# Kernel tuning notes

Hardware: AMD Instinct MI355X
Metric: run time of the kernel (lower is better)

## Reference

```python
import jax, jax.numpy as jnp
import numpy as np

N_STATE = 2048
N_HEAD = 16
HEAD_DIM = N_STATE // N_HEAD  # 128
ROPE_THETA = 10000.0


def setup_inputs() -> dict:
    key = jax.random.key(0)
    ks = jax.random.split(key, 8)
    B, S, D = 2, 2048, N_STATE
    scale = 1.0 / np.sqrt(D)
    x = jax.random.normal(ks[0], (B, S, D), dtype=jnp.float32)
    Wq = jax.random.normal(ks[1], (D, D), dtype=jnp.float32) * scale
    bq = jnp.zeros((D,), dtype=jnp.float32)
    Wk = jax.random.normal(ks[2], (D, D), dtype=jnp.float32) * scale  # key has no bias
    Wv = jax.random.normal(ks[3], (D, D), dtype=jnp.float32) * scale
    bv = jnp.zeros((D,), dtype=jnp.float32)
    Wo = jax.random.normal(ks[4], (D, D), dtype=jnp.float32) * scale
    bo = jnp.zeros((D,), dtype=jnp.float32)
    return {"x": x, "Wq": Wq, "bq": bq, "Wk": Wk, "Wv": Wv, "bv": bv, "Wo": Wo, "bo": bo}


def _rope(t, pos):
    # t: [B, S, H, hd]; torchtune-style interleaved rotary (pairs of adjacent dims)
    hd = t.shape[-1]
    inv_freq = 1.0 / (ROPE_THETA ** (jnp.arange(0, hd, 2, dtype=jnp.float32) / hd))  # [hd/2]
    ang = pos[:, None] * inv_freq[None, :]                    # [S, hd/2]
    cos = jnp.cos(ang)[None, :, None, :].astype(t.dtype)       # [1,S,1,hd/2]
    sin = jnp.sin(ang)[None, :, None, :].astype(t.dtype)
    t1 = t[..., 0::2]
    t2 = t[..., 1::2]
    rot = jnp.stack([t1 * cos - t2 * sin, t2 * cos + t1 * sin], axis=-1)
    return rot.reshape(t.shape)


def reference(x, Wq, bq, Wk, Wv, bv, Wo, bo):
    B, S, D = x.shape
    H, hd = N_HEAD, D // N_HEAD
    q = (x @ Wq.T + bq).reshape(B, S, H, hd)
    k = (x @ Wk.T).reshape(B, S, H, hd)
    v = (x @ Wv.T + bv).reshape(B, S, H, hd)
    pos = jnp.arange(S, dtype=jnp.float32)
    q = _rope(q, pos)
    k = _rope(k, pos)
    # [B,H,S,hd]
    q = q.transpose(0, 2, 1, 3)
    k = k.transpose(0, 2, 1, 3)
    v = v.transpose(0, 2, 1, 3)
    scale = 1.0 / jnp.sqrt(jnp.asarray(hd, dtype=x.dtype))
    scores = jnp.einsum('bhqd,bhkd->bhqk', q, k) * scale       # [B,H,S,S]
    causal = jnp.tril(jnp.ones((S, S), dtype=bool))
    scores = jnp.where(causal[None, None], scores, jnp.finfo(scores.dtype).min)
    probs = jax.nn.softmax(scores, axis=-1)
    a = jnp.einsum('bhqk,bhkd->bhqd', probs, v)                # [B,H,S,hd]
    a = a.transpose(0, 2, 1, 3).reshape(B, S, D)
    return a @ Wo.T + bo
```

## Files before the change

kernel.cpp:

```cpp
#include <hip/hip_runtime.h>
#include <stdint.h>

typedef float f32x4 __attribute__((ext_vector_type(4)));
typedef __bf16 bf16x8 __attribute__((ext_vector_type(8)));
typedef unsigned short us8 __attribute__((ext_vector_type(8)));
typedef unsigned short us4 __attribute__((ext_vector_type(4)));
typedef unsigned int u32;

#define MFMA16(A, B, C) __builtin_amdgcn_mfma_f32_16x16x32_bf16( \
    __builtin_bit_cast(bf16x8, (A)), __builtin_bit_cast(bf16x8, (B)), (C), 0, 0, 0)

__device__ __forceinline__ unsigned short f2bf(float f) {
  u32 u = __builtin_bit_cast(u32, f);
  u = u + 0x7fffu + ((u >> 16) & 1u);
  return (unsigned short)(u >> 16);
}
__device__ __forceinline__ float bf2f(unsigned short b) {
  u32 u = ((u32)b) << 16;
  return __builtin_bit_cast(float, u);
}
__device__ __forceinline__ void gload16(const void* g, void* lds) {
  __builtin_amdgcn_global_load_lds((const __attribute__((address_space(1))) u32*)g,
                                   (__attribute__((address_space(3))) u32*)lds, 16, 0, 0);
}

__global__ __launch_bounds__(256) void convert_all(
    const float* __restrict__ x, const float* __restrict__ wq, const float* __restrict__ wk,
    const float* __restrict__ wv, const float* __restrict__ wo,
    unsigned short* __restrict__ xb, unsigned short* __restrict__ wcat,
    unsigned short* __restrict__ wob) {
  int tid = blockIdx.x * 256 + threadIdx.x;
  int nth = gridDim.x * 256;
  const float* srcs[5] = {x, wq, wk, wv, wo};
  unsigned short* dsts[5] = {xb, wcat, wcat + 4194304, wcat + 8388608, wob};
  const int n4s[5] = {2097152, 1048576, 1048576, 1048576, 1048576};
#pragma unroll
  for (int sg = 0; sg < 5; ++sg) {
    const float4* s = (const float4*)srcs[sg];
    us4* d = (us4*)dsts[sg];
    int n4 = n4s[sg];
    for (int i = tid; i < n4; i += nth) {
      float4 v = s[i];
      us4 o;
      o[0] = f2bf(v.x); o[1] = f2bf(v.y); o[2] = f2bf(v.z); o[3] = f2bf(v.w);
      d[i] = o;
    }
  }
}

template <int EPI>
__global__ __launch_bounds__(512, 2) void gemm2(
    const unsigned short* __restrict__ A, const unsigned short* __restrict__ B,
    int nTN, int N,
    float* __restrict__ outF, const float* __restrict__ bias,
    unsigned short* __restrict__ qb, unsigned short* __restrict__ kb,
    unsigned short* __restrict__ vtb, const float* __restrict__ bq,
    const float* __restrict__ bv) {
  constexpr int K = 2048, KT = 64;
  __shared__ alignas(16) char L[4 * 24576];
  int bid = (int)blockIdx.x, nwg = (int)gridDim.x;
  {
    int qq = nwg >> 3;
    int xcd = bid & 7, idx = bid >> 3;
    bid = xcd * qq + idx;
  }
  int tm = bid / nTN, tn = bid % nTN;
  int t = (int)threadIdx.x, l = t & 63, w = t >> 6;
  int g = l >> 4, ln = l & 15;
  int wr = w >> 2, wc = w & 3;
  const unsigned short* Ab =
      A + (size_t)(tm * 128 + w * 16 + (l >> 2)) * K + (l & 3) * 8;
  const unsigned short* Bb =
      B + (size_t)(tn * 256 + w * 16 + (l >> 2)) * K + (l & 3) * 8;
  f32x4 acc[4][4] = {};

#define STAGE(tile) do {                                                      \
    char* Lb = L + ((tile) & 3) * 24576 + w * 1024;                           \
    int kc = (tile) * 32;                                                     \
    gload16(Ab + kc, Lb);                                \
    gload16(Bb + kc, Lb + 8192);                         \
    gload16(Bb + (size_t)128 * K + kc, Lb + 16384);      \
  } while (0)

#define GITER(kt, VM) do {                                                    \
    asm volatile("s_waitcnt vmcnt(" #VM ")" ::: "memory");                    \
    __builtin_amdgcn_s_barrier();                                             \
    __builtin_amdgcn_sched_barrier(0);                                        \
    asm volatile("" ::: "memory");                                            \
    if ((kt) + 3 < KT) STAGE((kt) + 3);                                       \
    const unsigned short* Lc = (const unsigned short*)(L + ((kt) & 3) * 24576); \
    us8 af[4], bfr[4];                                                        \
    _Pragma("unroll") for (int mf = 0; mf < 4; ++mf)                          \
      af[mf] = *(const us8*)&Lc[(wr * 64 + mf * 16 + ln) * 32 + g * 8];       \
    _Pragma("unroll") for (int nf = 0; nf < 4; ++nf)                          \
      bfr[nf] = *(const us8*)&Lc[4096 + (wc * 64 + nf * 16 + ln) * 32 + g * 8]; \
    __builtin_amdgcn_s_setprio(1);                                            \
    _Pragma("unroll") for (int mf = 0; mf < 4; ++mf)                          \
      _Pragma("unroll") for (int nf = 0; nf < 4; ++nf)                        \
        acc[mf][nf] = MFMA16(af[mf], bfr[nf], acc[mf][nf]);                   \
    __builtin_amdgcn_s_setprio(0);                                            \
  } while (0)

  STAGE(0); STAGE(1); STAGE(2);
#pragma unroll 1
  for (int kt = 0; kt < KT - 2; ++kt) GITER(kt, 6);
  GITER(KT - 2, 3);
  GITER(KT - 1, 0);
#undef STAGE
#undef GITER

  if (EPI == 1) {
#pragma unroll
    for (int mf = 0; mf < 4; ++mf)
#pragma unroll
      for (int nf = 0; nf < 4; ++nf) {
        int n = tn * 256 + wc * 64 + nf * 16 + ln;
        float bz = bias[n];
#pragma unroll
        for (int r = 0; r < 4; ++r) {
          int m = tm * 128 + wr * 64 + mf * 16 + g * 4 + r;
          outF[(size_t)m * N + n] = acc[mf][nf][r] + bz;
        }
      }
  } else {
#pragma unroll
    for (int mf = 0; mf < 4; ++mf)
#pragma unroll
      for (int nf = 0; nf < 4; ++nf) {
        int n6 = tn * 256 + wc * 64 + nf * 16 + ln;
        int sel = n6 >> 11, d = n6 & 2047, h = d >> 7, hd = d & 127;
        int m0 = tm * 128 + wr * 64 + mf * 16 + g * 4;
        int b = m0 >> 11, s0 = m0 & 2047;
        if (sel == 2) {
          float badd = bv[d];
          us4 pk;
#pragma unroll
          for (int r = 0; r < 4; ++r) pk[r] = f2bf(acc[mf][nf][r] + badd);
          *(us4*)&vtb[((size_t)(b * 16 + h) * 128 + hd) * 2048 + s0] = pk;
        } else {
          unsigned short* dst = sel ? kb : qb;
          float badd = sel ? 0.f : bq[d];
#pragma unroll
          for (int r = 0; r < 4; ++r)
            dst[((size_t)(b * 16 + h) * 2048 + (s0 + r)) * 128 + hd] =
                f2bf(acc[mf][nf][r] + badd);
        }
      }
  }
}

__global__ __launch_bounds__(256) void rope_k(u32* __restrict__ q, u32* __restrict__ k) {
  int idx = blockIdx.x * 256 + threadIdx.x;
  int i = idx & 63;
  int s = (idx >> 6) & 2047;
  float ang = (float)s * exp2f(-(float)i * 0.2076205059304703f);
  float sv, cv;
  sincosf(ang, &sv, &cv);
  u32 qu = q[idx];
  float a0 = bf2f((unsigned short)(qu & 0xffff)), a1 = bf2f((unsigned short)(qu >> 16));
  q[idx] = (u32)f2bf(a0 * cv - a1 * sv) | ((u32)f2bf(a1 * cv + a0 * sv) << 16);
  u32 ku = k[idx];
  float b0 = bf2f((unsigned short)(ku & 0xffff)), b1 = bf2f((unsigned short)(ku >> 16));
  k[idx] = (u32)f2bf(b0 * cv - b1 * sv) | ((u32)f2bf(b1 * cv + b0 * sv) << 16);
}

__global__ __launch_bounds__(512) void attn_k(
    const unsigned short* __restrict__ qg, const unsigned short* __restrict__ kg,
    const unsigned short* __restrict__ vtg, unsigned short* __restrict__ ab) {
  __shared__ alignas(16) unsigned short Kl[64 * 128];
  __shared__ alignas(16) unsigned short Vl[128 * 64];
  __shared__ alignas(16) unsigned short Pl[8][16 * 72];
  int bh = (int)blockIdx.x & 31;
  int pr = (int)blockIdx.x >> 5;
  int t = (int)threadIdx.x, l = t & 63, w = t >> 6;
  int g = l >> 4, ln = l & 15;
  int b = bh >> 4, h = bh & 15;
  const size_t bq0 = (size_t)bh * 2048 * 128;

#pragma unroll 1
  for (int half = 0; half < 2; ++half) {
    int qt = half ? 15 - pr : pr;
    int qbase = qt * 128;
    int qrow = qbase + w * 16 + ln;
    us8 qf[4];
#pragma unroll
    for (int kf = 0; kf < 4; ++kf)
      qf[kf] = *(const us8*)&qg[bq0 + (size_t)qrow * 128 + kf * 32 + g * 8];
    f32x4 o[8] = {};
    float mrow = -1e30f, lrow = 0.f;
    int nkt = (qbase >> 6) + 2;
#pragma unroll 1
    for (int kt = 0; kt < nkt; ++kt) {
      __syncthreads();
#pragma unroll
      for (int i = 0; i < 2; ++i) {
        int fb = i * 8192 + w * 1024;
        int flat = fb + l * 16;
        int row = flat >> 8, colb = flat & 255;
        int sc = colb ^ ((row & 7) << 4);
        gload16(kg + (bq0 + (size_t)(kt * 64 + row) * 128 + (sc >> 1)), (char*)Kl + fb);
        int rv = flat >> 7, cv2 = flat & 127;
        int scv = cv2 ^ ((rv & 7) << 4);
        gload16(vtg + (bq0 + (size_t)rv * 2048 + kt * 64 + (scv >> 1)), (char*)Vl + fb);
      }
      __syncthreads();
      f32x4 st[4];
#pragma unroll
      for (int kfr = 0; kfr < 4; ++kfr) {
        f32x4 acc = {};
        int row = kfr * 16 + ln;
        int swz = (row & 7) << 4;
#pragma unroll
        for (int kf = 0; kf < 4; ++kf) {
          us8 kfrag = *(const us8*)((const char*)Kl + row * 256 + ((kf * 64 + g * 16) ^ swz));
          acc = MFMA16(kfrag, qf[kf], acc);
        }
        st[kfr] = acc;
      }
      float pmax = -1e30f;
#pragma unroll
      for (int kfr = 0; kfr < 4; ++kfr)
#pragma unroll
        for (int r = 0; r < 4; ++r) {
          int key = kt * 64 + kfr * 16 + g * 4 + r;
          float sv = key <= qrow ? st[kfr][r] * 0.08838834764831845f : -1e30f;
          st[kfr][r] = sv;
          pmax = fmaxf(pmax, sv);
        }
      pmax = fmaxf(pmax, __shfl_xor(pmax, 16));
      pmax = fmaxf(pmax, __shfl_xor(pmax, 32));
      if (__ballot(pmax > mrow + 8.f)) {
        float mnew = pmax > mrow + 8.f ? pmax : mrow;
        float corr = exp2f((mrow - mnew) * 1.44269504f);
        mrow = mnew;
        lrow *= corr;
#pragma unroll
        for (int r = 0; r < 4; ++r) {
          float cr = __shfl(corr, g * 4 + r);
#pragma unroll
          for (int nf = 0; nf < 8; ++nf) o[nf][r] *= cr;
        }
      }
      float lsum = 0.f;
#pragma unroll
      for (int kfr = 0; kfr < 4; ++kfr) {
        us4 pk;
#pragma unroll
        for (int r = 0; r < 4; ++r) {
          float p = exp2f((st[kfr][r] - mrow) * 1.44269504f);
          lsum += p;
          pk[r] = f2bf(p);
        }
        *(us4*)&Pl[w][ln * 72 + kfr * 16 + g * 4] = pk;
      }
      lsum += __shfl_xor(lsum, 16);
      lsum += __shfl_xor(lsum, 32);
      lrow += lsum;
#pragma unroll
      for (int kf2 = 0; kf2 < 2; ++kf2) {
        us8 pa = *(const us8*)&Pl[w][ln * 72 + kf2 * 32 + g * 8];
#pragma unroll
        for (int nf = 0; nf < 8; ++nf) {
          int row = nf * 16 + ln;
          us8 vb = *(const us8*)((const char*)Vl + row * 128 +
                                 ((kf2 * 64 + g * 16) ^ ((row & 7) << 4)));
          o[nf] = MFMA16(pa, vb, o[nf]);
        }
      }
    }
    float invl = 1.f / lrow;
#pragma unroll
    for (int r = 0; r < 4; ++r) {
      float ir = __shfl(invl, g * 4 + r);
      int srow = qbase + w * 16 + g * 4 + r;
      size_t base = ((size_t)b * 2048 + srow) * 2048 + h * 128 + ln;
#pragma unroll
      for (int nf = 0; nf < 8; ++nf) ab[base + (size_t)nf * 16] = f2bf(o[nf][r] * ir);
    }
  }
}

extern "C" void kernel_launch(void* const* d_in, const int* in_sizes, int n_in,
                              void* d_out, int out_size, void* d_ws, size_t ws_size,
                              hipStream_t stream) {
  const float* x  = (const float*)d_in[0];
  const float* Wq = (const float*)d_in[1];
  const float* bq = (const float*)d_in[2];
  const float* Wk = (const float*)d_in[3];
  const float* Wv = (const float*)d_in[4];
  const float* bv = (const float*)d_in[5];
  const float* Wo = (const float*)d_in[6];
  const float* bo = (const float*)d_in[7];
  float* out = (float*)d_out;

  unsigned short* ws = (unsigned short*)d_ws;
  unsigned short* xb   = ws;
  unsigned short* wcat = xb + 8388608;
  unsigned short* wob  = wcat + 12582912;
  unsigned short* qb   = wob + 4194304;
  unsigned short* kb   = qb + 8388608;
  unsigned short* vtb  = kb + 8388608;

  convert_all<<<2048, 256, 0, stream>>>(x, Wq, Wk, Wv, Wo, xb, wcat, wob);
  gemm2<0><<<768, 512, 0, stream>>>(xb, wcat, 24, 6144,
                                    nullptr, nullptr, qb, kb, vtb, bq, bv);
  rope_k<<<16384, 256, 0, stream>>>((u32*)qb, (u32*)kb);
  attn_k<<<256, 512, 0, stream>>>(qb, kb, vtb, xb );
  gemm2<1><<<256, 512, 0, stream>>>(xb, wob, 8, 2048,
                                    out, bo, nullptr, nullptr, nullptr, nullptr, nullptr);
}
```

Before: 284.4 us.

## Rewrite GEMM as 256x256 tiles with 8-phase double-buffered LDS pipeline

Replaces the 128x256-tile GEMM with a 256x256-tile kernel using K=64 per stage, double-buffered 128KB LDS, and an 8-phase schedule interleaving half-tile global loads with MFMA sub-blocks. This raises arithmetic intensity per loaded byte and overlaps loads with compute at finer granularity. It halves the grid (384 and 128 blocks), which can reduce occupancy on 256 CUs, and the 128KB LDS limits each CU to one block despite the launch bounds.

```diff
diff --git a/kernel.cpp b/kernel.cpp
--- a/kernel.cpp
+++ b/kernel.cpp
@@ -49,15 +49,16 @@
 }
 
 template <int EPI>
-__global__ __launch_bounds__(512, 2) void gemm2(
+__global__ __launch_bounds__(512, 2) void gemm8(
     const unsigned short* __restrict__ A, const unsigned short* __restrict__ B,
     int nTN, int N,
     float* __restrict__ outF, const float* __restrict__ bias,
     unsigned short* __restrict__ qb, unsigned short* __restrict__ kb,
     unsigned short* __restrict__ vtb, const float* __restrict__ bq,
     const float* __restrict__ bv) {
-  constexpr int K = 2048, KT = 64;
-  __shared__ alignas(16) char L[4 * 24576];
+  constexpr int KT = 32;
+  __shared__ alignas(16) char L[131072];
+  char* Lp = L;
   int bid = (int)blockIdx.x, nwg = (int)gridDim.x;
   {
     int qq = nwg >> 3;
@@ -68,84 +69,120 @@
   int t = (int)threadIdx.x, l = t & 63, w = t >> 6;
   int g = l >> 4, ln = l & 15;
   int wr = w >> 2, wc = w & 3;
-  const unsigned short* Ab =
-      A + (size_t)(tm * 128 + w * 16 + (l >> 2)) * K + (l & 3) * 8;
-  const unsigned short* Bb =
-      B + (size_t)(tn * 256 + w * 16 + (l >> 2)) * K + (l & 3) * 8;
-  f32x4 acc[4][4] = {};
-
-#define STAGE(tile) do {                                                      \
-    char* Lb = L + ((tile) & 3) * 24576 + w * 1024;                           \
-    int kc = (tile) * 32;                                                     \
-    gload16(Ab + kc, Lb);                                \
-    gload16(Bb + kc, Lb + 8192);                         \
-    gload16(Bb + (size_t)128 * K + kc, Lb + 16384);      \
+  const unsigned short* pA = A + (size_t)(tm * 256 + l) * 2048 + w * 8;
+  const unsigned short* pB = B + (size_t)(tn * 256 + l) * 2048 + w * 8;
+
+  f32x4 acc[2][2][4][2] = {};
+  us8 af[4][2], bf[2][2];
+
+#define FENCE asm volatile("" ::: "memory")
+#define BAR do { FENCE; __builtin_amdgcn_s_barrier(); FENCE; } while (0)
+#define VMW_(n) asm volatile("s_waitcnt vmcnt(" #n ")" ::: "memory")
+#define VMW(n) VMW_(n)
+#define HT(op, h, kt, bufsel) do { if ((kt) < KT) {                           \
+    char* lb = Lp + (bufsel) * 65536 + (op) * 32768 + (h) * 16384 + w * 2048; \
+    const unsigned short* gs = ((op) ? pB : pA) +                             \
+        (size_t)((h) * 128) * 2048 + (size_t)(kt) * 64;                       \
+    gload16(gs, lb);                                                          \
+    gload16(gs + (size_t)64 * 2048, lb + 1024);                               \
+  } } while (0)
+#define RD_A(mh_, bufsel) do {                                                \
+    _Pragma("unroll") for (int mf = 0; mf < 4; ++mf)                          \
+    _Pragma("unroll") for (int kc = 0; kc < 2; ++kc)                          \
+      af[mf][kc] = *(const us8*)(Lp + (bufsel) * 65536 + wr * 16384 +         \
+          (kc * 4 + g) * 2048 + ((mh_) * 64 + mf * 16 + ln) * 16);            \
   } while (0)
-
-#define GITER(kt, VM) do {                                                    \
-    asm volatile("s_waitcnt vmcnt(" #VM ")" ::: "memory");                    \
-    __builtin_amdgcn_s_barrier();                                             \
-    __builtin_amdgcn_sched_barrier(0);                                        \
-    asm volatile("" ::: "memory");                                            \
-    if ((kt) + 3 < KT) STAGE((kt) + 3);                                       \
-    const unsigned short* Lc = (const unsigned short*)(L + ((kt) & 3) * 24576); \
-    us8 af[4], bfr[4];                                                        \
-    _Pragma("unroll") for (int mf = 0; mf < 4; ++mf)                          \
-      af[mf] = *(const us8*)&Lc[(wr * 64 + mf * 16 + ln) * 32 + g * 8];       \
-    _Pragma("unroll") for (int nf = 0; nf < 4; ++nf)                          \
-      bfr[nf] = *(const us8*)&Lc[4096 + (wc * 64 + nf * 16 + ln) * 32 + g * 8]; \
+#define RD_B(nh_, bufsel) do {                                                \
+    _Pragma("unroll") for (int nf = 0; nf < 2; ++nf)                          \
+    _Pragma("unroll") for (int kc = 0; kc < 2; ++kc)                          \
+      bf[nf][kc] = *(const us8*)(Lp + (bufsel) * 65536 + 32768 +              \
+          (wc >> 1) * 16384 + (kc * 4 + g) * 2048 +                           \
+          ((wc & 1) * 64 + (nh_) * 32 + nf * 16 + ln) * 16);                  \
+  } while (0)
+#define MM(mh_, nh_) do {                                                     \
     __builtin_amdgcn_s_setprio(1);                                            \
     _Pragma("unroll") for (int mf = 0; mf < 4; ++mf)                          \
-      _Pragma("unroll") for (int nf = 0; nf < 4; ++nf)                        \
-        acc[mf][nf] = MFMA16(af[mf], bfr[nf], acc[mf][nf]);                   \
+    _Pragma("unroll") for (int nf = 0; nf < 2; ++nf)                          \
+    _Pragma("unroll") for (int kc = 0; kc < 2; ++kc)                          \
+      acc[mh_][nh_][mf][nf] = MFMA16(af[mf][kc], bf[nf][kc],                  \
+                                     acc[mh_][nh_][mf][nf]);                  \
     __builtin_amdgcn_s_setprio(0);                                            \
   } while (0)
-
-  STAGE(0); STAGE(1); STAGE(2);
+#define ITER(k0, VM3) do { int k1_ = (k0) + 1;                                \
+   RD_A(0, 0); RD_B(0, 0); HT(0, 1, k1_, 1);     BAR; MM(0, 0); BAR;   \
+   RD_B(1, 0);             HT(1, 0, k1_, 1);     BAR; MM(0, 1); BAR;   \
+   RD_A(1, 0);             HT(1, 1, k1_, 1);     BAR; MM(1, 1); BAR;   \
+   RD_B(0, 0);             HT(0, 0, (k0) + 2, 0); BAR; MM(1, 0);       \
+          VMW(VM3); BAR;                                                      \
+   RD_A(0, 1); RD_B(0, 1); HT(0, 1, (k0) + 2, 0); BAR; MM(0, 0); BAR;  \
+   RD_B(1, 1);             HT(1, 0, (k0) + 2, 0); BAR; MM(0, 1); BAR;  \
+   RD_A(1, 1);             HT(1, 1, (k0) + 2, 0); BAR; MM(1, 1); BAR;  \
+   RD_B(0, 1);             HT(0, 0, k1_ + 2, 1);  BAR; MM(1, 0);       \
+          VMW(2); BAR;                                                        \
+} while (0)
+
+  HT(0, 0, 0, 0); HT(0, 1, 0, 0); HT(1, 0, 0, 0); HT(1, 1, 0, 0);
+  HT(0, 0, 1, 1);
+  VMW(2); BAR;
+
 #pragma unroll 1
-  for (int kt = 0; kt < KT - 2; ++kt) GITER(kt, 6);
-  GITER(KT - 2, 3);
-  GITER(KT - 1, 0);
-#undef STAGE
-#undef GITER
+  for (int it = 0; it < 15; ++it) ITER(2 * it, 2);
+  ITER(30, 0);
+
+#undef ITER
+#undef MM
+#undef RD_B
+#undef RD_A
+#undef HT
+#undef VMW
+#undef VMW_
+#undef BAR
+#undef FENCE
 
   if (EPI == 1) {
 #pragma unroll
+    for (int mh = 0; mh < 2; ++mh)
+#pragma unroll
+    for (int nh = 0; nh < 2; ++nh)
+#pragma unroll
     for (int mf = 0; mf < 4; ++mf)
 #pragma unroll
-      for (int nf = 0; nf < 4; ++nf) {
-        int n = tn * 256 + wc * 64 + nf * 16 + ln;
-        float bz = bias[n];
-#pragma unroll
-        for (int r = 0; r < 4; ++r) {
-          int m = tm * 128 + wr * 64 + mf * 16 + g * 4 + r;
-          outF[(size_t)m * N + n] = acc[mf][nf][r] + bz;
-        }
-      }
+    for (int nf = 0; nf < 2; ++nf) {
+      int n = tn * 256 + wc * 64 + nh * 32 + nf * 16 + ln;
+      float bz = bias[n];
+      int m0 = tm * 256 + wr * 128 + mh * 64 + mf * 16 + g * 4;
+#pragma unroll
+      for (int r = 0; r < 4; ++r)
+        outF[(size_t)(m0 + r) * N + n] = acc[mh][nh][mf][nf][r] + bz;
+    }
   } else {
 #pragma unroll
+    for (int mh = 0; mh < 2; ++mh)
+#pragma unroll
+    for (int nh = 0; nh < 2; ++nh)
+#pragma unroll
     for (int mf = 0; mf < 4; ++mf)
 #pragma unroll
-      for (int nf = 0; nf < 4; ++nf) {
-        int n6 = tn * 256 + wc * 64 + nf * 16 + ln;
-        int sel = n6 >> 11, d = n6 & 2047, h = d >> 7, hd = d & 127;
-        int m0 = tm * 128 + wr * 64 + mf * 16 + g * 4;
-        int b = m0 >> 11, s0 = m0 & 2047;
-        if (sel == 2) {
-          float badd = bv[d];
-          us4 pk;
-#pragma unroll
-          for (int r = 0; r < 4; ++r) pk[r] = f2bf(acc[mf][nf][r] + badd);
-          *(us4*)&vtb[((size_t)(b * 16 + h) * 128 + hd) * 2048 + s0] = pk;
-        } else {
-          unsigned short* dst = sel ? kb : qb;
-          float badd = sel ? 0.f : bq[d];
-#pragma unroll
-          for (int r = 0; r < 4; ++r)
-            dst[((size_t)(b * 16 + h) * 2048 + (s0 + r)) * 128 + hd] =
-                f2bf(acc[mf][nf][r] + badd);
-        }
-      }
+    for (int nf = 0; nf < 2; ++nf) {
+      int n6 = tn * 256 + wc * 64 + nh * 32 + nf * 16 + ln;
+      int sel = n6 >> 11, d = n6 & 2047, h = d >> 7, hd = d & 127;
+      int m0 = tm * 256 + wr * 128 + mh * 64 + mf * 16 + g * 4;
+      int b = m0 >> 11, s0 = m0 & 2047;
+      if (sel == 2) {
+        float badd = bv[d];
+        us4 pk;
+#pragma unroll
+        for (int r = 0; r < 4; ++r) pk[r] = f2bf(acc[mh][nh][mf][nf][r] + badd);
+        *(us4*)&vtb[((size_t)(b * 16 + h) * 128 + hd) * 2048 + s0] = pk;
+      } else {
+        unsigned short* dst = sel ? kb : qb;
+        float badd = sel ? 0.f : bq[d];
+#pragma unroll
+        for (int r = 0; r < 4; ++r)
+          dst[((size_t)(b * 16 + h) * 2048 + (s0 + r)) * 128 + hd] =
+              f2bf(acc[mh][nh][mf][nf][r] + badd);
+      }
+    }
   }
 }
 
@@ -302,10 +339,10 @@
   unsigned short* vtb  = kb + 8388608;
 
   convert_all<<<2048, 256, 0, stream>>>(x, Wq, Wk, Wv, Wo, xb, wcat, wob);
-  gemm2<0><<<768, 512, 0, stream>>>(xb, wcat, 24, 6144,
+  gemm8<0><<<384, 512, 0, stream>>>(xb, wcat, 24, 6144,
                                     nullptr, nullptr, qb, kb, vtb, bq, bv);
   rope_k<<<16384, 256, 0, stream>>>((u32*)qb, (u32*)kb);
   attn_k<<<256, 512, 0, stream>>>(qb, kb, vtb, xb );
-  gemm2<1><<<256, 512, 0, stream>>>(xb, wob, 8, 2048,
+  gemm8<1><<<128, 512, 0, stream>>>(xb, wob, 8, 2048,
                                     out, bo, nullptr, nullptr, nullptr, nullptr, nullptr);
 }
```

After: 328.8 us. +15.6%, slower.

## Use 32x32x16 MFMA with triple-buffered LDS for QKV projection GEMM

Applied to the files above, without the earlier changes.

Adds a new QKV GEMM kernel built on 32x32x16 bf16 MFMAs with 16-wide accumulators. It uses a new LDS layout split into two k-halves, three LDS buffers instead of four, and the wait and barrier moved to the end of each iteration. Launch bounds rise to four blocks per CU. The aim is fewer LDS reads per FLOP and higher MFMA throughput, plus more occupancy from the smaller LDS footprint. The old gemm2 is kept only for the output projection, with its QKV epilogue removed. The new loading and indexing scheme raises the risk of LDS bank conflicts and layout errors.

```diff
diff --git a/kernel.cpp b/kernel.cpp
--- a/kernel.cpp
+++ b/kernel.cpp
@@ -2,12 +2,15 @@
 #include <stdint.h>
 
 typedef float f32x4 __attribute__((ext_vector_type(4)));
+typedef float f32x16 __attribute__((ext_vector_type(16)));
 typedef __bf16 bf16x8 __attribute__((ext_vector_type(8)));
 typedef unsigned short us8 __attribute__((ext_vector_type(8)));
 typedef unsigned short us4 __attribute__((ext_vector_type(4)));
 typedef unsigned int u32;
 
 #define MFMA16(A, B, C) __builtin_amdgcn_mfma_f32_16x16x32_bf16( \
+    __builtin_bit_cast(bf16x8, (A)), __builtin_bit_cast(bf16x8, (B)), (C), 0, 0, 0)
+#define MFMA32(A, B, C) __builtin_amdgcn_mfma_f32_32x32x16_bf16( \
     __builtin_bit_cast(bf16x8, (A)), __builtin_bit_cast(bf16x8, (B)), (C), 0, 0, 0)
 
 __device__ __forceinline__ unsigned short f2bf(float f) {
@@ -49,13 +52,136 @@
 }
 
 template <int EPI>
-__global__ __launch_bounds__(512, 2) void gemm2(
+__global__ __launch_bounds__(512, 4) void gemm32(
     const unsigned short* __restrict__ A, const unsigned short* __restrict__ B,
     int nTN, int N,
     float* __restrict__ outF, const float* __restrict__ bias,
     unsigned short* __restrict__ qb, unsigned short* __restrict__ kb,
     unsigned short* __restrict__ vtb, const float* __restrict__ bq,
     const float* __restrict__ bv) {
+  constexpr int KT = 64;
+  __shared__ alignas(16) char L[3 * 24576];
+  char* Lp = L;
+  int bid = (int)blockIdx.x, nwg = (int)gridDim.x;
+  {
+    int qq = nwg >> 3;
+    int xcd = bid & 7, idx = bid >> 3;
+    bid = xcd * qq + idx;
+  }
+  int tm = bid / nTN, tn = bid % nTN;
+  int t = (int)threadIdx.x, l = t & 63, w = t >> 6;
+  int hi = l >> 5, l31 = l & 31;
+  int wr = w >> 2, wc = w & 3;
+  const unsigned short* pAl =
+      A + (size_t)(tm * 128 + (w & 1) * 64 + l) * 2048 + (w >> 1) * 8;
+  const unsigned short* pB0 =
+      B + (size_t)(tn * 256 + ((2 * w) & 3) * 64 + l) * 2048 + ((2 * w) >> 2) * 8;
+  const unsigned short* pB1 =
+      B + (size_t)(tn * 256 + ((2 * w + 1) & 3) * 64 + l) * 2048 + ((2 * w + 1) >> 2) * 8;
+  const int dA = w * 1024;
+  const int dB0 = 8192 + (2 * w) * 1024;
+  const int dB1 = 8192 + (2 * w + 1) * 1024;
+  const int aoff = hi * 2048 + (wr * 64 + l31) * 16;
+  const int boff = 8192 + hi * 4096 + (wc * 64 + l31) * 16;
+
+  f32x16 acc[2][2] = {};
+
+#define STG(kt, bufs) do { if ((kt) < KT) {                                   \
+    int kc_ = (kt) * 32;                                                      \
+    gload16(pAl + kc_, Lp + (bufs) * 24576 + dA);                             \
+    gload16(pB0 + kc_, Lp + (bufs) * 24576 + dB0);                            \
+    gload16(pB1 + kc_, Lp + (bufs) * 24576 + dB1);                            \
+  } } while (0)
+
+#define GITER(kt, bufc, bufs, VM) do {                                        \
+    STG((kt) + 2, bufs);                                                      \
+    us8 af[2][2], bfr[2][2];                                                  \
+    _Pragma("unroll") for (int kc = 0; kc < 2; ++kc) {                        \
+      _Pragma("unroll") for (int mh = 0; mh < 2; ++mh)                        \
+        af[kc][mh] = *(const us8*)(Lp + (bufc) * 24576 + kc * 4096 +          \
+                                   mh * 512 + aoff);                          \
+      _Pragma("unroll") for (int nh = 0; nh < 2; ++nh)                        \
+        bfr[kc][nh] = *(const us8*)(Lp + (bufc) * 24576 + kc * 8192 +         \
+                                    nh * 512 + boff);                         \
+    }                                                                         \
+    __builtin_amdgcn_s_setprio(1);                                            \
+    _Pragma("unroll") for (int kc = 0; kc < 2; ++kc)                          \
+    _Pragma("unroll") for (int mh = 0; mh < 2; ++mh)                          \
+    _Pragma("unroll") for (int nh = 0; nh < 2; ++nh)                          \
+      acc[mh][nh] = MFMA32(af[kc][mh], bfr[kc][nh], acc[mh][nh]);             \
+    __builtin_amdgcn_s_setprio(0);                                            \
+    asm volatile("s_waitcnt vmcnt(" #VM ")" ::: "memory");                    \
+    __builtin_amdgcn_s_barrier();                                             \
+    asm volatile("" ::: "memory");                                            \
+  } while (0)
+
+  STG(0, 0); STG(1, 1);
+  asm volatile("s_waitcnt vmcnt(3)" ::: "memory");
+  __builtin_amdgcn_s_barrier();
+  asm volatile("" ::: "memory");
+
+#pragma unroll 1
+  for (int t3 = 0; t3 < 60; t3 += 3) {
+    GITER(t3 + 0, 0, 2, 3);
+    GITER(t3 + 1, 1, 0, 3);
+    GITER(t3 + 2, 2, 1, 3);
+  }
+  GITER(60, 0, 2, 3);
+  GITER(61, 1, 0, 3);
+  GITER(62, 2, 1, 0);
+  GITER(63, 0, 2, 0);
+
+#undef GITER
+#undef STG
+
+#pragma unroll
+  for (int mh = 0; mh < 2; ++mh)
+#pragma unroll
+  for (int nh = 0; nh < 2; ++nh) {
+    int mb = tm * 128 + wr * 64 + mh * 32 + 4 * hi;
+    if (EPI == 1) {
+      int n = tn * 256 + wc * 64 + nh * 32 + l31;
+      float bz = bias[n];
+#pragma unroll
+      for (int q = 0; q < 4; ++q)
+#pragma unroll
+        for (int j = 0; j < 4; ++j)
+          outF[(size_t)(mb + 8 * q + j) * N + n] = acc[mh][nh][4 * q + j] + bz;
+    } else {
+      int n6 = tn * 256 + wc * 64 + nh * 32 + l31;
+      int sel = n6 >> 11, d = n6 & 2047, h = d >> 7, hd = d & 127;
+      int b = mb >> 11;
+      if (sel == 2) {
+        float badd = bv[d];
+#pragma unroll
+        for (int q = 0; q < 4; ++q) {
+          int s0 = (mb + 8 * q) & 2047;
+          us4 pk;
+#pragma unroll
+          for (int j = 0; j < 4; ++j) pk[j] = f2bf(acc[mh][nh][4 * q + j] + badd);
+          *(us4*)&vtb[((size_t)(b * 16 + h) * 128 + hd) * 2048 + s0] = pk;
+        }
+      } else {
+        unsigned short* dst = sel ? kb : qb;
+        float badd = sel ? 0.f : bq[d];
+#pragma unroll
+        for (int q = 0; q < 4; ++q) {
+          int s0 = (mb + 8 * q) & 2047;
+#pragma unroll
+          for (int j = 0; j < 4; ++j)
+            dst[((size_t)(b * 16 + h) * 2048 + (s0 + j)) * 128 + hd] =
+                f2bf(acc[mh][nh][4 * q + j] + badd);
+        }
+      }
+    }
+  }
+}
+
+template <int EPI>
+__global__ __launch_bounds__(512, 2) void gemm2(
+    const unsigned short* __restrict__ A, const unsigned short* __restrict__ B,
+    int nTN, int N,
+    float* __restrict__ outF, const float* __restrict__ bias) {
   constexpr int K = 2048, KT = 64;
   __shared__ alignas(16) char L[4 * 24576];
   int bid = (int)blockIdx.x, nwg = (int)gridDim.x;
@@ -77,9 +203,9 @@
 #define STAGE(tile) do {                                                      \
     char* Lb = L + ((tile) & 3) * 24576 + w * 1024;                           \
     int kc = (tile) * 32;                                                     \
-    gload16(Ab + kc, Lb);                                \
-    gload16(Bb + kc, Lb + 8192);                         \
-    gload16(Bb + (size_t)128 * K + kc, Lb + 16384);      \
+    gload16(Ab + kc, Lb);                                                     \
+    gload16(Bb + kc, Lb + 8192);                                              \
+    gload16(Bb + (size_t)128 * K + kc, Lb + 16384);                           \
   } while (0)
 
 #define GITER(kt, VM) do {                                                    \
@@ -109,44 +235,18 @@
 #undef STAGE
 #undef GITER
 
-  if (EPI == 1) {
-#pragma unroll
-    for (int mf = 0; mf < 4; ++mf)
-#pragma unroll
-      for (int nf = 0; nf < 4; ++nf) {
-        int n = tn * 256 + wc * 64 + nf * 16 + ln;
-        float bz = bias[n];
-#pragma unroll
-        for (int r = 0; r < 4; ++r) {
-          int m = tm * 128 + wr * 64 + mf * 16 + g * 4 + r;
-          outF[(size_t)m * N + n] = acc[mf][nf][r] + bz;
-        }
-      }
-  } else {
-#pragma unroll
-    for (int mf = 0; mf < 4; ++mf)
-#pragma unroll
-      for (int nf = 0; nf < 4; ++nf) {
-        int n6 = tn * 256 + wc * 64 + nf * 16 + ln;
-        int sel = n6 >> 11, d = n6 & 2047, h = d >> 7, hd = d & 127;
-        int m0 = tm * 128 + wr * 64 + mf * 16 + g * 4;
-        int b = m0 >> 11, s0 = m0 & 2047;
-        if (sel == 2) {
-          float badd = bv[d];
-          us4 pk;
-#pragma unroll
-          for (int r = 0; r < 4; ++r) pk[r] = f2bf(acc[mf][nf][r] + badd);
-          *(us4*)&vtb[((size_t)(b * 16 + h) * 128 + hd) * 2048 + s0] = pk;
-        } else {
-          unsigned short* dst = sel ? kb : qb;
-          float badd = sel ? 0.f : bq[d];
-#pragma unroll
-          for (int r = 0; r < 4; ++r)
-            dst[((size_t)(b * 16 + h) * 2048 + (s0 + r)) * 128 + hd] =
-                f2bf(acc[mf][nf][r] + badd);
-        }
-      }
-  }
+#pragma unroll
+  for (int mf = 0; mf < 4; ++mf)
+#pragma unroll
+    for (int nf = 0; nf < 4; ++nf) {
+      int n = tn * 256 + wc * 64 + nf * 16 + ln;
+      float bz = bias[n];
+#pragma unroll
+      for (int r = 0; r < 4; ++r) {
+        int m = tm * 128 + wr * 64 + mf * 16 + g * 4 + r;
+        outF[(size_t)m * N + n] = acc[mf][nf][r] + bz;
+      }
+    }
 }
 
 __global__ __launch_bounds__(256) void rope_k(u32* __restrict__ q, u32* __restrict__ k) {
@@ -302,10 +402,9 @@
   unsigned short* vtb  = kb + 8388608;
 
   convert_all<<<2048, 256, 0, stream>>>(x, Wq, Wk, Wv, Wo, xb, wcat, wob);
-  gemm2<0><<<768, 512, 0, stream>>>(xb, wcat, 24, 6144,
-                                    nullptr, nullptr, qb, kb, vtb, bq, bv);
+  gemm32<0><<<768, 512, 0, stream>>>(xb, wcat, 24, 6144,
+                                     nullptr, nullptr, qb, kb, vtb, bq, bv);
   rope_k<<<16384, 256, 0, stream>>>((u32*)qb, (u32*)kb);
   attn_k<<<256, 512, 0, stream>>>(qb, kb, vtb, xb );
-  gemm2<1><<<256, 512, 0, stream>>>(xb, wob, 8, 2048,
-                                    out, bo, nullptr, nullptr, nullptr, nullptr, nullptr);
-}
+  gemm2<1><<<256, 512, 0, stream>>>(xb, wob, 8, 2048, out, bo);
+}
```

Measured after the change: 346.9 us. +22.0%, slower.
